# Performance work log

Measured on AMD Instinct MI355X. Metric: run time of the kernel, lower is better.

## Reference

```python
import jax, jax.numpy as jnp
import numpy as np

N = 100000  # nodes
E = 1600000  # directed edges

_DIMS = [("eg1", 3, 160), ("eg2", 160, 80), ("eg3", 80, 40), ("eg4", 40, 20),
         ("el1", 20, 10), ("el2", 10, 3), ("dl1", 3, 10), ("dl2", 10, 20),
         ("dg1", 20, 40), ("dg2", 40, 80), ("dg3", 80, 160), ("dg4", 160, 3)]


def _lin_init(key, ci, co):
    s = 1.0 / np.sqrt(ci)
    kw, kb = jax.random.split(key)
    w = jax.random.uniform(kw, (ci, co), jnp.float32, -s, s)
    b = jax.random.uniform(kb, (co,), jnp.float32, -s, s)
    return w, b


def setup_inputs():
    key = jax.random.key(0)
    k0, k1, k2 = jax.random.split(key, 3)
    x = jax.random.normal(k0, (N, 3), jnp.float32)
    src = jax.random.randint(k1, (E,), 0, N)
    dst = jax.random.randint(k2, (E,), 0, N)
    edge_index = jnp.stack([src, dst])  # [2, E] int32 indices
    out = {"x": x, "edge_index": edge_index}
    for i, (name, ci, co) in enumerate(_DIMS):
        w, b = _lin_init(jax.random.fold_in(key, i + 10), ci, co)
        out[name + "_w"] = w
        out[name + "_b"] = b
    return out


def _gcn(x, w, b, src, dst, norm):
    # PyG GCNConv: linear transform, then symmetric-normalized scatter-add.
    h = x @ w
    agg = jax.ops.segment_sum(h[src] * norm[:, None], dst, num_segments=N)
    return agg + b


def reference(x, edge_index, eg1_w, eg1_b, eg2_w, eg2_b, eg3_w, eg3_b, eg4_w, eg4_b,
              el1_w, el1_b, el2_w, el2_b, dl1_w, dl1_b, dl2_w, dl2_b,
              dg1_w, dg1_b, dg2_w, dg2_b, dg3_w, dg3_b, dg4_w, dg4_b):
    loops = jnp.arange(N)
    src = jnp.concatenate([edge_index[0], loops])  # add self-loops (PyG default)
    dst = jnp.concatenate([edge_index[1], loops])
    deg = jax.ops.segment_sum(jnp.ones(src.shape[0], x.dtype), dst, num_segments=N)
    dis = jnp.where(deg > 0, jax.lax.rsqrt(deg), 0.0)
    norm = dis[src] * dis[dst]  # D^-1/2 A D^-1/2 edge weights
    relu = jax.nn.relu
    h = relu(_gcn(x, eg1_w, eg1_b, src, dst, norm))
    h = relu(_gcn(h, eg2_w, eg2_b, src, dst, norm))
    h = relu(_gcn(h, eg3_w, eg3_b, src, dst, norm))
    h = relu(_gcn(h, eg4_w, eg4_b, src, dst, norm))
    h = relu(h @ el1_w + el1_b)
    h = h @ el2_w + el2_b  # latent [N, 3]
    h = relu(h @ dl1_w + dl1_b)
    h = relu(h @ dl2_w + dl2_b)
    h = relu(_gcn(h, dg1_w, dg1_b, src, dst, norm))
    h = relu(_gcn(h, dg2_w, dg2_b, src, dst, norm))
    h = relu(_gcn(h, dg3_w, dg3_b, src, dst, norm))
    h = jnp.tanh(_gcn(h, dg4_w, dg4_b, src, dst, norm))
    return h
```

## Files before the change

### kernel.cpp

```cpp
#include <hip/hip_runtime.h>
#include <hip/hip_fp16.h>
#include <math.h>

#define BS 256
static constexpr int NN = 100000;
static constexpr int EE = 1600000;
static constexpr int BUCKET_SH = 7;
static constexpr int NBUCKET = (NN + 127) >> BUCKET_SH;
static constexpr int NB_PART = 256;
static constexpr int CHUNK = EE / NB_PART;
static constexpr int NP_ = NBUCKET * NB_PART;
static constexpr int SCAN_ELEMS = 1024;
static constexpr int NPB = (NP_ + SCAN_ELEMS - 1) / SCAN_ELEMS;

static inline int cdiv(long long a, int b) { return (int)((a + b - 1) / b); }

typedef _Float16 half8 __attribute__((ext_vector_type(8)));
typedef float f32x4 __attribute__((ext_vector_type(4)));

template <int ACT>
__device__ __forceinline__ float act_f(float v) {
    if (ACT == 1) return fmaxf(v, 0.0f);
    if (ACT == 2) return tanhf(v);
    return v;
}

__device__ __forceinline__ unsigned short h16(float v) {
    return __half_as_ushort(__float2half(v));
}
__device__ __forceinline__ unsigned pack2h(float a, float b) {
    return (unsigned)h16(a) | ((unsigned)h16(b) << 16);
}
__device__ __forceinline__ float4 cvt4h(uint2 r) {
    float2 fa = __half22float2(*(const __half2*)&r.x);
    float2 fb = __half22float2(*(const __half2*)&r.y);
    return make_float4(fa.x, fa.y, fb.x, fb.y);
}
__device__ __forceinline__ void acc8h(uint4 r, float4& a, float4& b) {
    float2 f0 = __half22float2(*(const __half2*)&r.x);
    float2 f1 = __half22float2(*(const __half2*)&r.y);
    float2 f2 = __half22float2(*(const __half2*)&r.z);
    float2 f3 = __half22float2(*(const __half2*)&r.w);
    a.x += f0.x; a.y += f0.y; a.z += f1.x; a.w += f1.y;
    b.x += f2.x; b.y += f2.y; b.z += f3.x; b.w += f3.y;
}

template <int OUTM>
__device__ __forceinline__ void store1(float* out, size_t idx, float v, float dn) {
    if (OUTM == 0) out[idx] = v;
    else if (OUTM == 1) out[idx] = v * dn;
    else if (OUTM == 2) ((unsigned short*)out)[idx] = h16(v * dn);
    else ((unsigned short*)out)[idx] = h16(v);
}

__global__ __launch_bounds__(256) void k_hist(const int* __restrict__ dst,
                                              int* __restrict__ part_cnt) {
    __shared__ int h[NBUCKET];
    int b = blockIdx.x;
    for (int j = threadIdx.x; j < NBUCKET; j += 256) h[j] = 0;
    __syncthreads();
    int e0 = b * CHUNK;
    for (int k = threadIdx.x; k < CHUNK; k += 256)
        atomicAdd(&h[dst[e0 + k] >> BUCKET_SH], 1);
    __syncthreads();
    for (int j = threadIdx.x; j < NBUCKET; j += 256)
        part_cnt[j * NB_PART + b] = h[j];
}

__global__ void k_scanA(const int* __restrict__ in, int* __restrict__ outp,
                        int* __restrict__ bsums) {
    __shared__ int lds[BS];
    int base = blockIdx.x * SCAN_ELEMS;
    int t = threadIdx.x;
    int v[4];
    int s = 0;
#pragma unroll
    for (int j = 0; j < 4; ++j) {
        int idx = base + t * 4 + j;
        v[j] = (idx < NP_) ? in[idx] : 0;
        s += v[j];
    }
    lds[t] = s;
    __syncthreads();
    for (int off = 1; off < BS; off <<= 1) {
        int add = (t >= off) ? lds[t - off] : 0;
        __syncthreads();
        lds[t] += add;
        __syncthreads();
    }
    int run = lds[t] - s;
    if (t == BS - 1) bsums[blockIdx.x] = lds[BS - 1];
#pragma unroll
    for (int j = 0; j < 4; ++j) {
        int idx = base + t * 4 + j;
        if (idx < NP_) outp[idx] = run;
        run += v[j];
    }
}

__global__ void k_scanB(int* __restrict__ bsums) {
    if (threadIdx.x == 0 && blockIdx.x == 0) {
        int acc = 0;
        for (int i = 0; i < NPB; ++i) {
            int t = bsums[i];
            bsums[i] = acc;
            acc += t;
        }
    }
}

__global__ void k_scanC(int* __restrict__ outp, const int* __restrict__ bsums,
                        int* __restrict__ bbase) {
    int i = blockIdx.x * BS + threadIdx.x;
    if (i < NP_) {
        int v = outp[i] + bsums[i / SCAN_ELEMS];
        outp[i] = v;
        if ((i & (NB_PART - 1)) == 0) bbase[i / NB_PART] = v;
    }
    if (i == 0) bbase[NBUCKET] = EE;
}

__global__ __launch_bounds__(256) void k_part(const int* __restrict__ src,
                                              const int* __restrict__ dst,
                                              const int* __restrict__ scan_out,
                                              unsigned* __restrict__ epb) {
    __shared__ int cur[NBUCKET];
    int b = blockIdx.x;
    for (int j = threadIdx.x; j < NBUCKET; j += 256) cur[j] = scan_out[j * NB_PART + b];
    __syncthreads();
    int e0 = b * CHUNK;
    for (int k = threadIdx.x; k < CHUNK; k += 256) {
        int e = e0 + k;
        int d = dst[e];
        int s = src[e];
        int pos = atomicAdd(&cur[d >> BUCKET_SH], 1);
        epb[pos] = ((unsigned)(d & ((1 << BUCKET_SH) - 1)) << 17) | (unsigned)s;
    }
}

__global__ __launch_bounds__(256) void k_fine2(const int* __restrict__ bbase,
                                               const unsigned* __restrict__ epb,
                                               int* __restrict__ eidx,
                                               int* __restrict__ rowptr,
                                               float* __restrict__ dis) {
    __shared__ int hcnt[1 << BUCKET_SH];
    __shared__ int hoff[1 << BUCKET_SH];
    int b = blockIdx.x;
    int n0 = b << BUCKET_SH;
    int nloc = min(1 << BUCKET_SH, NN - n0);
    int t = threadIdx.x;
    if (t < (1 << BUCKET_SH)) hcnt[t] = 0;
    __syncthreads();
    int es = bbase[b], ee = bbase[b + 1];
    for (int k = es + t; k < ee; k += 256) atomicAdd(&hcnt[epb[k] >> 17], 1);
    __syncthreads();
    if (t < (1 << BUCKET_SH)) hoff[t] = hcnt[t];
    __syncthreads();
    for (int off = 1; off < (1 << BUCKET_SH); off <<= 1) {
        int add = (t >= off && t < (1 << BUCKET_SH)) ? hoff[t - off] : 0;
        __syncthreads();
        if (t < (1 << BUCKET_SH)) hoff[t] += add;
        __syncthreads();
    }
    if (t < nloc) {
        int excl = hoff[t] - hcnt[t];
        rowptr[n0 + t] = es + excl;
        dis[n0 + t] = rsqrtf((float)(hcnt[t] + 1));
    }
    __syncthreads();
    if (t < (1 << BUCKET_SH)) hoff[t] = es + hoff[t] - hcnt[t];
    __syncthreads();
    for (int k = es + t; k < ee; k += 256) {
        unsigned p = epb[k];
        int pos = atomicAdd(&hoff[p >> 17], 1);
        eidx[pos] = (int)(p & 0x1FFFFu);
    }
    if (b == NBUCKET - 1 && t == 0) rowptr[NN] = EE;
}

template <int C, int ACT, bool HASB, bool OUTH>
__global__ void k_gatherw(const unsigned short* __restrict__ g, const int* __restrict__ rowptr,
                          const int* __restrict__ eidx, const float* __restrict__ dis,
                          const float* __restrict__ b, float* __restrict__ out) {
    static_assert(C % 8 == 0, "C%8");
    constexpr int V = C / 8;
    int t = blockIdx.x * BS + threadIdx.x;
    if (t >= NN * V) return;
    int n = t / V, v = t % V;
    const uint4* g4 = (const uint4*)g;
    float4 accA = make_float4(0.f, 0.f, 0.f, 0.f);
    float4 accB = make_float4(0.f, 0.f, 0.f, 0.f);
    acc8h(g4[(size_t)n * V + v], accA, accB);
    int rs = rowptr[n], re = rowptr[n + 1];
    int k = rs;
    for (; k + 4 <= re; k += 4) {
        int s0 = eidx[k + 0], s1 = eidx[k + 1], s2 = eidx[k + 2], s3 = eidx[k + 3];
        uint4 r0 = g4[(size_t)s0 * V + v];
        uint4 r1 = g4[(size_t)s1 * V + v];
        uint4 r2 = g4[(size_t)s2 * V + v];
        uint4 r3 = g4[(size_t)s3 * V + v];
        acc8h(r0, accA, accB);
        acc8h(r1, accA, accB);
        acc8h(r2, accA, accB);
        acc8h(r3, accA, accB);
    }
    for (; k < re; ++k) {
        acc8h(g4[(size_t)eidx[k] * V + v], accA, accB);
    }
    float dn = dis[n];
    accA.x *= dn; accA.y *= dn; accA.z *= dn; accA.w *= dn;
    accB.x *= dn; accB.y *= dn; accB.z *= dn; accB.w *= dn;
    if (HASB) {
        float4 b0 = ((const float4*)b)[v * 2 + 0];
        float4 b1 = ((const float4*)b)[v * 2 + 1];
        accA.x += b0.x; accA.y += b0.y; accA.z += b0.z; accA.w += b0.w;
        accB.x += b1.x; accB.y += b1.y; accB.z += b1.z; accB.w += b1.w;
    }
    accA.x = act_f<ACT>(accA.x); accA.y = act_f<ACT>(accA.y);
    accA.z = act_f<ACT>(accA.z); accA.w = act_f<ACT>(accA.w);
    accB.x = act_f<ACT>(accB.x); accB.y = act_f<ACT>(accB.y);
    accB.z = act_f<ACT>(accB.z); accB.w = act_f<ACT>(accB.w);
    if (OUTH) {
        uint4 u;
        u.x = pack2h(accA.x, accA.y);
        u.y = pack2h(accA.z, accA.w);
        u.z = pack2h(accB.x, accB.y);
        u.w = pack2h(accB.z, accB.w);
        ((uint4*)out)[(size_t)n * V + v] = u;
    } else {
        float4* op = (float4*)out + (size_t)n * (C / 4) + v * 2;
        op[0] = accA;
        op[1] = accB;
    }
}

template <int C, int ACT, bool HASB, bool OUTH>
__global__ void k_gatherh(const unsigned short* __restrict__ g, const int* __restrict__ rowptr,
                          const int* __restrict__ eidx, const float* __restrict__ dis,
                          const float* __restrict__ b, float* __restrict__ out) {
    static_assert(C % 4 == 0, "C%4");
    constexpr int V = C / 4;
    int t = blockIdx.x * BS + threadIdx.x;
    if (t >= NN * V) return;
    int n = t / V, v = t % V;
    const uint2* g2 = (const uint2*)g;
    float4 acc = cvt4h(g2[(size_t)n * V + v]);
    int rs = rowptr[n], re = rowptr[n + 1];
    int k = rs;
    for (; k + 4 <= re; k += 4) {
        int s0 = eidx[k + 0], s1 = eidx[k + 1], s2 = eidx[k + 2], s3 = eidx[k + 3];
        uint2 r0 = g2[(size_t)s0 * V + v];
        uint2 r1 = g2[(size_t)s1 * V + v];
        uint2 r2 = g2[(size_t)s2 * V + v];
        uint2 r3 = g2[(size_t)s3 * V + v];
        float4 h0 = cvt4h(r0), h1 = cvt4h(r1), h2 = cvt4h(r2), h3 = cvt4h(r3);
        acc.x += (h0.x + h1.x) + (h2.x + h3.x);
        acc.y += (h0.y + h1.y) + (h2.y + h3.y);
        acc.z += (h0.z + h1.z) + (h2.z + h3.z);
        acc.w += (h0.w + h1.w) + (h2.w + h3.w);
    }
    for (; k < re; ++k) {
        float4 hv = cvt4h(g2[(size_t)eidx[k] * V + v]);
        acc.x += hv.x; acc.y += hv.y; acc.z += hv.z; acc.w += hv.w;
    }
    float dn = dis[n];
    acc.x *= dn; acc.y *= dn; acc.z *= dn; acc.w *= dn;
    if (HASB) {
        float4 bb = ((const float4*)b)[v];
        acc.x += bb.x; acc.y += bb.y; acc.z += bb.z; acc.w += bb.w;
    }
    acc.x = act_f<ACT>(acc.x);
    acc.y = act_f<ACT>(acc.y);
    acc.z = act_f<ACT>(acc.z);
    acc.w = act_f<ACT>(acc.w);
    if (OUTH) {
        uint2 u;
        u.x = pack2h(acc.x, acc.y);
        u.y = pack2h(acc.z, acc.w);
        ((uint2*)out)[(size_t)n * V + v] = u;
    } else {
        ((float4*)out)[(size_t)n * V + v] = acc;
    }
}

template <int ACT, bool HASB>
__global__ void k_gather3d(const float* __restrict__ g, const int* __restrict__ rowptr,
                           const int* __restrict__ eidx, const float* __restrict__ dis,
                           const float* __restrict__ b, float* __restrict__ out) {
    int n = blockIdx.x * BS + threadIdx.x;
    if (n >= NN) return;
    const float* gp = g + (size_t)n * 3;
    float a0 = gp[0], a1 = gp[1], a2 = gp[2];
    int rs = rowptr[n], re = rowptr[n + 1];
    int k = rs;
    for (; k + 4 <= re; k += 4) {
        const float* q0 = g + (size_t)eidx[k + 0] * 3;
        const float* q1 = g + (size_t)eidx[k + 1] * 3;
        const float* q2 = g + (size_t)eidx[k + 2] * 3;
        const float* q3 = g + (size_t)eidx[k + 3] * 3;
        float b00 = q0[0], b01 = q0[1], b02 = q0[2];
        float b10 = q1[0], b11 = q1[1], b12 = q1[2];
        float b20 = q2[0], b21 = q2[1], b22 = q2[2];
        float b30 = q3[0], b31 = q3[1], b32 = q3[2];
        a0 += (b00 + b10) + (b20 + b30);
        a1 += (b01 + b11) + (b21 + b31);
        a2 += (b02 + b12) + (b22 + b32);
    }
    for (; k < re; ++k) {
        const float* gq = g + (size_t)eidx[k] * 3;
        a0 += gq[0]; a1 += gq[1]; a2 += gq[2];
    }
    float dn = dis[n];
    a0 *= dn; a1 *= dn; a2 *= dn;
    if (HASB) { a0 += b[0]; a1 += b[1]; a2 += b[2]; }
    float* op = out + (size_t)n * 3;
    op[0] = act_f<ACT>(a0);
    op[1] = act_f<ACT>(a1);
    op[2] = act_f<ACT>(a2);
}

__global__ void k_scale3(const float* __restrict__ x, const float* __restrict__ dis,
                         float* __restrict__ g) {
    int i = blockIdx.x * BS + threadIdx.x;
    if (i < NN * 3) g[i] = x[i] * dis[i / 3];
}

__global__ __launch_bounds__(256) void k_latent(const unsigned short* __restrict__ in20,
                                                const float* __restrict__ el1_w, const float* __restrict__ el1_b,
                                                const float* __restrict__ el2_w, const float* __restrict__ el2_b,
                                                const float* __restrict__ dl1_w, const float* __restrict__ dl1_b,
                                                const float* __restrict__ dl2_w, const float* __restrict__ dl2_b,
                                                const float* __restrict__ dis,
                                                unsigned short* __restrict__ G) {
    __shared__ float w1[200], b1[10], w2[30], b2[3], w3[30], b3[10], w4[200], b4[20];
    int t = threadIdx.x;
    if (t < 200) w1[t] = el1_w[t];
    if (t < 10) b1[t] = el1_b[t];
    if (t < 30) w2[t] = el2_w[t];
    if (t < 3) b2[t] = el2_b[t];
    if (t < 30) w3[t] = dl1_w[t];
    if (t < 10) b3[t] = dl1_b[t];
    if (t < 200) w4[t] = dl2_w[t];
    if (t < 20) b4[t] = dl2_b[t];
    __syncthreads();
    int n = blockIdx.x * 256 + t;
    if (n >= NN) return;
    float h0[20];
    const uint2* ip = (const uint2*)in20 + (size_t)n * 5;
#pragma unroll
    for (int v = 0; v < 5; ++v) {
        float4 f = cvt4h(ip[v]);
        h0[v * 4 + 0] = f.x; h0[v * 4 + 1] = f.y;
        h0[v * 4 + 2] = f.z; h0[v * 4 + 3] = f.w;
    }
    float a1[10];
#pragma unroll
    for (int j = 0; j < 10; ++j) {
        float s = b1[j];
#pragma unroll
        for (int i = 0; i < 20; ++i) s = fmaf(h0[i], w1[i * 10 + j], s);
        a1[j] = fmaxf(s, 0.0f);
    }
    float a2[3];
#pragma unroll
    for (int j = 0; j < 3; ++j) {
        float s = b2[j];
#pragma unroll
        for (int i = 0; i < 10; ++i) s = fmaf(a1[i], w2[i * 3 + j], s);
        a2[j] = s;
    }
    float a3[10];
#pragma unroll
    for (int j = 0; j < 10; ++j) {
        float s = b3[j];
#pragma unroll
        for (int i = 0; i < 3; ++i) s = fmaf(a2[i], w3[i * 10 + j], s);
        a3[j] = fmaxf(s, 0.0f);
    }
    float dn = dis[n];
    uint2* gp = (uint2*)G + (size_t)n * 5;
#pragma unroll
    for (int v = 0; v < 5; ++v) {
        float o[4];
#pragma unroll
        for (int q = 0; q < 4; ++q) {
            int j = v * 4 + q;
            float s = b4[j];
#pragma unroll
            for (int i = 0; i < 10; ++i) s = fmaf(a3[i], w4[i * 20 + j], s);
            o[q] = fmaxf(s, 0.0f) * dn;
        }
        uint2 u;
        u.x = pack2h(o[0], o[1]);
        u.y = pack2h(o[2], o[3]);
        gp[v] = u;
    }
}

template <int K, int N>
__global__ void k_wprep(const float* __restrict__ w, _Float16* __restrict__ wh) {
    constexpr int KP = (K + 31) & ~31;
    constexpr int NT = (N + 15) / 16;
    constexpr int NPAD = NT * 16;
    int i = blockIdx.x * 256 + threadIdx.x;
    if (i >= KP * NPAD) return;
    int k = i / NPAD, n = i % NPAD;
    float v = (k < K && n < N) ? w[k * N + n] : 0.0f;
    wh[((size_t)(k >> 3) * NPAD + n) * 8 + (k & 7)] = (_Float16)v;
}

template <int K, int N, int ACT, bool HASB, int OUTM>
__global__ __launch_bounds__(256) void k_mfma(const unsigned short* __restrict__ x,
                                              const _Float16* __restrict__ wh,
                                              const float* __restrict__ bias,
                                              unsigned short* __restrict__ out,
                                              const float* __restrict__ dis) {
    static_assert(K % 8 == 0, "K%8");
    constexpr int KP = (K + 31) & ~31;
    constexpr int KC = KP / 32;
    constexpr int NT = (N + 15) / 16;
    constexpr int NPAD = NT * 16;
    const int wid = blockIdx.x * 4 + (threadIdx.x >> 6);
    const int lane = threadIdx.x & 63;
    const int lm = lane & 15;
    const int quad = lane >> 4;
    const int arow = wid * 16 + lm;

    f32x4 acc[NT];
#pragma unroll
    for (int t = 0; t < NT; ++t) acc[t] = (f32x4){0.f, 0.f, 0.f, 0.f};

    const _Float16* xr = (const _Float16*)x + (size_t)arow * K;
#pragma unroll
    for (int kc = 0; kc < KC; ++kc) {
        int k0 = kc * 32 + quad * 8;
        half8 a = (half8)(_Float16)0;
        if (arow < NN && k0 < K) a = *(const half8*)(xr + k0);
#pragma unroll
        for (int t = 0; t < NT; ++t) {
            half8 bf = *(const half8*)&wh[((size_t)(kc * 4 + quad) * NPAD + t * 16 + lm) * 8];
            acc[t] = __builtin_amdgcn_mfma_f32_16x16x32_f16(a, bf, acc[t], 0, 0, 0);
        }
    }

    float bb[NT];
#pragma unroll
    for (int t = 0; t < NT; ++t) {
        int col = t * 16 + lm;
        bb[t] = (HASB && col < N) ? bias[col] : 0.0f;
    }
#pragma unroll
    for (int r = 0; r < 4; ++r) {
        int orow = wid * 16 + quad * 4 + r;
        if (orow < NN) {
            float dn = (OUTM == 2) ? dis[orow] : 1.0f;
#pragma unroll
            for (int t = 0; t < NT; ++t) {
                int col = t * 16 + lm;
                if (col < N) {
                    float v = act_f<ACT>(acc[t][r] + bb[t]);
                    if (OUTM == 2) v *= dn;
                    out[(size_t)orow * N + col] = h16(v);
                }
            }
        }
    }
}

template <int CIN, int COUT, int ACT, int OUTM>
__global__ void k_mm_rowbcast(const float* __restrict__ x, const float* __restrict__ w,
                              const float* __restrict__ b, float* __restrict__ out) {
    static_assert(COUT % 4 == 0, "c4");
    constexpr int COUT4 = COUT / 4;
    int i = blockIdx.x * BS + threadIdx.x;
    if (i >= NN * COUT4) return;
    int n = i / COUT4, c4 = i % COUT4;
    const float4* w4 = (const float4*)w;
    float4 acc = ((const float4*)b)[c4];
    const float* xr = x + (size_t)n * CIN;
#pragma unroll
    for (int ci = 0; ci < CIN; ++ci) {
        float xv = xr[ci];
        float4 wv = w4[ci * COUT4 + c4];
        acc.x = fmaf(xv, wv.x, acc.x);
        acc.y = fmaf(xv, wv.y, acc.y);
        acc.z = fmaf(xv, wv.z, acc.z);
        acc.w = fmaf(xv, wv.w, acc.w);
    }
    acc.x = act_f<ACT>(acc.x); acc.y = act_f<ACT>(acc.y);
    acc.z = act_f<ACT>(acc.z); acc.w = act_f<ACT>(acc.w);
    if (OUTM == 3) {
        uint2 u;
        u.x = pack2h(acc.x, acc.y);
        u.y = pack2h(acc.z, acc.w);
        ((uint2*)out)[(size_t)n * COUT4 + c4] = u;
    } else {
        ((float4*)out)[(size_t)n * COUT4 + c4] = acc;
    }
}

template <int CIN, int COUT, int ACT, bool HASB, int OUTM, bool INH>
__global__ void k_mm_vec4(const float* __restrict__ x, const float* __restrict__ w,
                          const float* __restrict__ b, float* __restrict__ out,
                          const float* __restrict__ dis) {
    static_assert(CIN % 4 == 0 && COUT % 4 == 0, "align");
    constexpr int TM = 8;
    constexpr int CIN4 = CIN / 4;
    constexpr int COUT4 = COUT / 4;
    constexpr int RG = NN / TM;
    int i = blockIdx.x * BS + threadIdx.x;
    if (i >= RG * COUT4) return;
    int c4 = i % COUT4;
    int n0 = (i / COUT4) * TM;
    const float4* x4 = (const float4*)x;
    const uint2* xh = (const uint2*)x;
    const float4* w4 = (const float4*)w;
    float4 acc[TM];
    float4 bb = HASB ? ((const float4*)b)[c4] : make_float4(0.f, 0.f, 0.f, 0.f);
#pragma unroll
    for (int r = 0; r < TM; ++r) acc[r] = bb;
    for (int k4 = 0; k4 < CIN4; ++k4) {
        float4 wv[4];
#pragma unroll
        for (int j = 0; j < 4; ++j) wv[j] = w4[(size_t)(4 * k4 + j) * COUT4 + c4];
#pragma unroll
        for (int r = 0; r < TM; ++r) {
            float4 xv;
            if (INH) xv = cvt4h(xh[(size_t)(n0 + r) * CIN4 + k4]);
            else xv = x4[(size_t)(n0 + r) * CIN4 + k4];
            acc[r].x = fmaf(xv.x, wv[0].x, fmaf(xv.y, wv[1].x, fmaf(xv.z, wv[2].x, fmaf(xv.w, wv[3].x, acc[r].x))));
            acc[r].y = fmaf(xv.x, wv[0].y, fmaf(xv.y, wv[1].y, fmaf(xv.z, wv[2].y, fmaf(xv.w, wv[3].y, acc[r].y))));
            acc[r].z = fmaf(xv.x, wv[0].z, fmaf(xv.y, wv[1].z, fmaf(xv.z, wv[2].z, fmaf(xv.w, wv[3].z, acc[r].z))));
            acc[r].w = fmaf(xv.x, wv[0].w, fmaf(xv.y, wv[1].w, fmaf(xv.z, wv[2].w, fmaf(xv.w, wv[3].w, acc[r].w))));
        }
    }
#pragma unroll
    for (int r = 0; r < TM; ++r) {
        float vx = act_f<ACT>(acc[r].x), vy = act_f<ACT>(acc[r].y);
        float vz = act_f<ACT>(acc[r].z), vw = act_f<ACT>(acc[r].w);
        size_t gi = (size_t)(n0 + r) * COUT4 + c4;
        if (OUTM == 2) {
            float dn = dis[n0 + r];
            uint2 u;
            u.x = pack2h(vx * dn, vy * dn);
            u.y = pack2h(vz * dn, vw * dn);
            ((uint2*)out)[gi] = u;
        } else if (OUTM == 1) {
            float dn = dis[n0 + r];
            ((float4*)out)[gi] = make_float4(vx * dn, vy * dn, vz * dn, vw * dn);
        } else {
            ((float4*)out)[gi] = make_float4(vx, vy, vz, vw);
        }
    }
}

template <int CIN, int COUT, int ACT, bool HASB, int OUTM, bool INH>
__global__ void k_mm_vec(const float* __restrict__ x, const float* __restrict__ w,
                         const float* __restrict__ b, float* __restrict__ out,
                         const float* __restrict__ dis) {
    static_assert(CIN % 4 == 0, "CIN%4");
    constexpr int TM = 8;
    constexpr int CIN4 = CIN / 4;
    constexpr int RG = NN / TM;
    int i = blockIdx.x * BS + threadIdx.x;
    if (i >= RG * COUT) return;
    int c = i % COUT;
    int n0 = (i / COUT) * TM;
    float acc[TM];
    float bb = HASB ? b[c] : 0.0f;
#pragma unroll
    for (int r = 0; r < TM; ++r) acc[r] = bb;
    const float4* x4 = (const float4*)x;
    const uint2* xh = (const uint2*)x;
    for (int k = 0; k < CIN4; ++k) {
        float w0 = w[(4 * k + 0) * COUT + c];
        float w1 = w[(4 * k + 1) * COUT + c];
        float w2 = w[(4 * k + 2) * COUT + c];
        float w3 = w[(4 * k + 3) * COUT + c];
#pragma unroll
        for (int r = 0; r < TM; ++r) {
            float4 xv;
            if (INH) xv = cvt4h(xh[(size_t)(n0 + r) * CIN4 + k]);
            else xv = x4[(size_t)(n0 + r) * CIN4 + k];
            acc[r] = fmaf(xv.x, w0, fmaf(xv.y, w1, fmaf(xv.z, w2, fmaf(xv.w, w3, acc[r]))));
        }
    }
#pragma unroll
    for (int r = 0; r < TM; ++r) {
        int row = n0 + r;
        float dn = (OUTM == 1 || OUTM == 2) ? dis[row] : 0.0f;
        store1<OUTM>(out, (size_t)row * COUT + c, act_f<ACT>(acc[r]), dn);
    }
}

extern "C" void kernel_launch(void* const* d_in, const int* in_sizes, int n_in,
                              void* d_out, int out_size, void* d_ws, size_t ws_size,
                              hipStream_t stream) {
    const float* x = (const float*)d_in[0];
    const int* ei = (const int*)d_in[1];
    const int* src = ei;
    const int* dst = ei + EE;
    const float* eg1_w = (const float*)d_in[2];  const float* eg1_b = (const float*)d_in[3];
    const float* eg2_w = (const float*)d_in[4];  const float* eg2_b = (const float*)d_in[5];
    const float* eg3_w = (const float*)d_in[6];  const float* eg3_b = (const float*)d_in[7];
    const float* eg4_w = (const float*)d_in[8];  const float* eg4_b = (const float*)d_in[9];
    const float* el1_w = (const float*)d_in[10]; const float* el1_b = (const float*)d_in[11];
    const float* el2_w = (const float*)d_in[12]; const float* el2_b = (const float*)d_in[13];
    const float* dl1_w = (const float*)d_in[14]; const float* dl1_b = (const float*)d_in[15];
    const float* dl2_w = (const float*)d_in[16]; const float* dl2_b = (const float*)d_in[17];
    const float* dg1_w = (const float*)d_in[18]; const float* dg1_b = (const float*)d_in[19];
    const float* dg2_w = (const float*)d_in[20]; const float* dg2_b = (const float*)d_in[21];
    const float* dg3_w = (const float*)d_in[22]; const float* dg3_b = (const float*)d_in[23];
    const float* dg4_w = (const float*)d_in[24]; const float* dg4_b = (const float*)d_in[25];
    float* out = (float*)d_out;

    char* ws = (char*)d_ws;
    size_t off = 0;
    auto alloc = [&](size_t bytes) {
        void* p = ws + off;
        off += (bytes + 15) & ~(size_t)15;
        return p;
    };
    int* part_cnt = (int*)alloc(sizeof(int) * NP_);
    int* scan_out = (int*)alloc(sizeof(int) * NP_);
    int* bsums    = (int*)alloc(sizeof(int) * NPB);
    int* bbase    = (int*)alloc(sizeof(int) * (NBUCKET + 1));
    int* rowptr   = (int*)alloc(sizeof(int) * (NN + 1));
    float* dis    = (float*)alloc(sizeof(float) * NN);
    int* eidx     = (int*)alloc(sizeof(int) * EE);
    unsigned* epb = (unsigned*)alloc(sizeof(unsigned) * EE);
    unsigned short* G = (unsigned short*)alloc(sizeof(unsigned short) * 80 * (size_t)NN);
    float* bufA = (float*)alloc(sizeof(float) * 160 * (size_t)NN);
    float* bufB = (float*)alloc(sizeof(float) * 160 * (size_t)NN);
    _Float16* whEg2 = (_Float16*)alloc(sizeof(_Float16) * (160 / 8) * 80 * 8);
    _Float16* whEg3 = (_Float16*)alloc(sizeof(_Float16) * (96 / 8) * 48 * 8);
    _Float16* whDg2 = (_Float16*)alloc(sizeof(_Float16) * (64 / 8) * 80 * 8);
    _Float16* whDg3 = (_Float16*)alloc(sizeof(_Float16) * (96 / 8) * 160 * 8);

    k_hist<<<NB_PART, 256, 0, stream>>>(dst, part_cnt);
    k_scanA<<<NPB, BS, 0, stream>>>(part_cnt, scan_out, bsums);
    k_scanB<<<1, 64, 0, stream>>>(bsums);
    k_scanC<<<cdiv(NP_, BS), BS, 0, stream>>>(scan_out, bsums, bbase);
    k_part<<<NB_PART, 256, 0, stream>>>(src, dst, scan_out, epb);
    k_fine2<<<NBUCKET, 256, 0, stream>>>(bbase, epb, eidx, rowptr, dis);

    k_wprep<160, 80><<<cdiv(160 * 80, 256), 256, 0, stream>>>(eg2_w, whEg2);
    k_wprep<80, 40><<<cdiv(96 * 48, 256), 256, 0, stream>>>(eg3_w, whEg3);
    k_wprep<40, 80><<<cdiv(64 * 80, 256), 256, 0, stream>>>(dg2_w, whDg2);
    k_wprep<80, 160><<<cdiv(96 * 160, 256), 256, 0, stream>>>(dg3_w, whDg3);

    k_scale3<<<cdiv(3LL * NN, BS), BS, 0, stream>>>(x, dis, bufB);
    k_gather3d<0, false><<<cdiv(NN, BS), BS, 0, stream>>>(bufB, rowptr, eidx, dis, nullptr, bufA);
    k_mm_rowbcast<3, 160, 1, 3><<<cdiv(NN * 40LL, BS), BS, 0, stream>>>(bufA, eg1_w, eg1_b, bufB);

    k_mfma<160, 80, 0, false, 2><<<cdiv(NN, 64), 256, 0, stream>>>(
        (const unsigned short*)bufB, whEg2, nullptr, G, dis);
    k_gatherw<80, 1, true, true><<<cdiv(NN * 10LL, BS), BS, 0, stream>>>(G, rowptr, eidx, dis, eg2_b, bufA);

    k_mfma<80, 40, 0, false, 2><<<cdiv(NN, 64), 256, 0, stream>>>(
        (const unsigned short*)bufA, whEg3, nullptr, G, dis);
    k_gatherw<40, 1, true, true><<<cdiv(NN * 5LL, BS), BS, 0, stream>>>(G, rowptr, eidx, dis, eg3_b, bufB);

    k_mm_vec4<40, 20, 0, false, 2, true><<<cdiv((NN / 8) * 5LL, BS), BS, 0, stream>>>(
        bufB, eg4_w, nullptr, (float*)G, dis);
    k_gatherh<20, 1, true, true><<<cdiv(NN * 5LL, BS), BS, 0, stream>>>(G, rowptr, eidx, dis, eg4_b, bufA);

    k_latent<<<cdiv(NN, 256), 256, 0, stream>>>((const unsigned short*)bufA,
        el1_w, el1_b, el2_w, el2_b, dl1_w, dl1_b, dl2_w, dl2_b, dis, G);

    k_gatherh<20, 0, false, true><<<cdiv(NN * 5LL, BS), BS, 0, stream>>>(G, rowptr, eidx, dis, nullptr, bufA);
    k_mm_vec4<20, 40, 1, true, 2, true><<<cdiv((NN / 8) * 10LL, BS), BS, 0, stream>>>(
        bufA, dg1_w, dg1_b, (float*)G, dis);

    k_gatherw<40, 0, false, true><<<cdiv(NN * 5LL, BS), BS, 0, stream>>>(G, rowptr, eidx, dis, nullptr, bufB);
    k_mfma<40, 80, 1, true, 2><<<cdiv(NN, 64), 256, 0, stream>>>(
        (const unsigned short*)bufB, whDg2, dg2_b, G, dis);

    k_gatherw<80, 0, false, true><<<cdiv(NN * 10LL, BS), BS, 0, stream>>>(G, rowptr, eidx, dis, nullptr, bufA);
    k_mfma<80, 160, 1, true, 3><<<cdiv(NN, 64), 256, 0, stream>>>(
        (const unsigned short*)bufA, whDg3, dg3_b, (unsigned short*)bufB, nullptr);

    k_mm_vec<160, 3, 0, false, 1, true><<<cdiv((NN / 8) * 3LL, BS), BS, 0, stream>>>(bufB, dg4_w, nullptr, bufA, dis);
    k_gather3d<2, true><<<cdiv(NN, BS), BS, 0, stream>>>(bufA, rowptr, eidx, dis, dg4_b, out);
}
```

Measured before the change: 527.4 us.

## Fuse neighbor gathers with following matmuls into combined per-layer kernels

```diff
diff --git a/kernel.cpp b/kernel.cpp
--- a/kernel.cpp
+++ b/kernel.cpp
@@ -43,6 +43,19 @@
     float2 f3 = __half22float2(*(const __half2*)&r.w);
     a.x += f0.x; a.y += f0.y; a.z += f1.x; a.w += f1.y;
     b.x += f2.x; b.y += f2.y; b.z += f3.x; b.w += f3.y;
+}
+__device__ __forceinline__ void addrow8(uint4 r, float* h) {
+    float2 f0 = __half22float2(*(const __half2*)&r.x);
+    float2 f1 = __half22float2(*(const __half2*)&r.y);
+    float2 f2 = __half22float2(*(const __half2*)&r.z);
+    float2 f3 = __half22float2(*(const __half2*)&r.w);
+    h[0] += f0.x; h[1] += f0.y; h[2] += f1.x; h[3] += f1.y;
+    h[4] += f2.x; h[5] += f2.y; h[6] += f3.x; h[7] += f3.y;
+}
+__device__ __forceinline__ void addrow4(uint2 r, float* h) {
+    float2 f0 = __half22float2(*(const __half2*)&r.x);
+    float2 f1 = __half22float2(*(const __half2*)&r.y);
+    h[0] += f0.x; h[1] += f0.y; h[2] += f1.x; h[3] += f1.y;
 }
 
 template <int OUTM>
@@ -178,109 +191,54 @@
     if (b == NBUCKET - 1 && t == 0) rowptr[NN] = EE;
 }
 
-template <int C, int ACT, bool HASB, bool OUTH>
-__global__ void k_gatherw(const unsigned short* __restrict__ g, const int* __restrict__ rowptr,
-                          const int* __restrict__ eidx, const float* __restrict__ dis,
-                          const float* __restrict__ b, float* __restrict__ out) {
-    static_assert(C % 8 == 0, "C%8");
-    constexpr int V = C / 8;
-    int t = blockIdx.x * BS + threadIdx.x;
-    if (t >= NN * V) return;
-    int n = t / V, v = t % V;
-    const uint4* g4 = (const uint4*)g;
-    float4 accA = make_float4(0.f, 0.f, 0.f, 0.f);
-    float4 accB = make_float4(0.f, 0.f, 0.f, 0.f);
-    acc8h(g4[(size_t)n * V + v], accA, accB);
+template <int K, int N>
+__device__ __forceinline__ void wconv(const float* __restrict__ w, _Float16* __restrict__ wh, int i) {
+    constexpr int NT = (N + 15) / 16;
+    constexpr int NPAD = NT * 16;
+    int k = i / NPAD, n = i % NPAD;
+    float v = (k < K && n < N) ? w[k * N + n] : 0.0f;
+    wh[((size_t)(k >> 3) * NPAD + n) * 8 + (k & 7)] = (_Float16)v;
+}
+
+__global__ void k_wprep_all(const float* __restrict__ w1, const float* __restrict__ w2,
+                            const float* __restrict__ w3, const float* __restrict__ w4,
+                            _Float16* __restrict__ o1, _Float16* __restrict__ o2,
+                            _Float16* __restrict__ o3, _Float16* __restrict__ o4) {
+    int i = blockIdx.x * 256 + threadIdx.x;
+    if (i < 12800) wconv<160, 80>(w1, o1, i);
+    else if (i < 17408) wconv<80, 40>(w2, o2, i - 12800);
+    else if (i < 22528) wconv<40, 80>(w3, o3, i - 17408);
+    else if (i < 37888) wconv<80, 160>(w4, o4, i - 22528);
+}
+
+__global__ void k_gather3x(const float* __restrict__ x, const int* __restrict__ rowptr,
+                           const int* __restrict__ eidx, const float* __restrict__ dis,
+                           float* __restrict__ out) {
+    int n = blockIdx.x * BS + threadIdx.x;
+    if (n >= NN) return;
+    float dn = dis[n];
+    float a0 = x[(size_t)n * 3 + 0] * dn;
+    float a1 = x[(size_t)n * 3 + 1] * dn;
+    float a2 = x[(size_t)n * 3 + 2] * dn;
     int rs = rowptr[n], re = rowptr[n + 1];
     int k = rs;
-    for (; k + 4 <= re; k += 4) {
-        int s0 = eidx[k + 0], s1 = eidx[k + 1], s2 = eidx[k + 2], s3 = eidx[k + 3];
-        uint4 r0 = g4[(size_t)s0 * V + v];
-        uint4 r1 = g4[(size_t)s1 * V + v];
-        uint4 r2 = g4[(size_t)s2 * V + v];
-        uint4 r3 = g4[(size_t)s3 * V + v];
-        acc8h(r0, accA, accB);
-        acc8h(r1, accA, accB);
-        acc8h(r2, accA, accB);
-        acc8h(r3, accA, accB);
+    for (; k + 2 <= re; k += 2) {
+        int s0 = eidx[k], s1 = eidx[k + 1];
+        float d0 = dis[s0], d1 = dis[s1];
+        const float* q0 = x + (size_t)s0 * 3;
+        const float* q1 = x + (size_t)s1 * 3;
+        a0 += q0[0] * d0 + q1[0] * d1;
+        a1 += q0[1] * d0 + q1[1] * d1;
+        a2 += q0[2] * d0 + q1[2] * d1;
     }
     for (; k < re; ++k) {
-        acc8h(g4[(size_t)eidx[k] * V + v], accA, accB);
-    }
-    float dn = dis[n];
-    accA.x *= dn; accA.y *= dn; accA.z *= dn; accA.w *= dn;
-    accB.x *= dn; accB.y *= dn; accB.z *= dn; accB.w *= dn;
-    if (HASB) {
-        float4 b0 = ((const float4*)b)[v * 2 + 0];
-        float4 b1 = ((const float4*)b)[v * 2 + 1];
-        accA.x += b0.x; accA.y += b0.y; accA.z += b0.z; accA.w += b0.w;
-        accB.x += b1.x; accB.y += b1.y; accB.z += b1.z; accB.w += b1.w;
-    }
-    accA.x = act_f<ACT>(accA.x); accA.y = act_f<ACT>(accA.y);
-    accA.z = act_f<ACT>(accA.z); accA.w = act_f<ACT>(accA.w);
-    accB.x = act_f<ACT>(accB.x); accB.y = act_f<ACT>(accB.y);
-    accB.z = act_f<ACT>(accB.z); accB.w = act_f<ACT>(accB.w);
-    if (OUTH) {
-        uint4 u;
-        u.x = pack2h(accA.x, accA.y);
-        u.y = pack2h(accA.z, accA.w);
-        u.z = pack2h(accB.x, accB.y);
-        u.w = pack2h(accB.z, accB.w);
-        ((uint4*)out)[(size_t)n * V + v] = u;
-    } else {
-        float4* op = (float4*)out + (size_t)n * (C / 4) + v * 2;
-        op[0] = accA;
-        op[1] = accB;
-    }
-}
-
-template <int C, int ACT, bool HASB, bool OUTH>
-__global__ void k_gatherh(const unsigned short* __restrict__ g, const int* __restrict__ rowptr,
-                          const int* __restrict__ eidx, const float* __restrict__ dis,
-                          const float* __restrict__ b, float* __restrict__ out) {
-    static_assert(C % 4 == 0, "C%4");
-    constexpr int V = C / 4;
-    int t = blockIdx.x * BS + threadIdx.x;
-    if (t >= NN * V) return;
-    int n = t / V, v = t % V;
-    const uint2* g2 = (const uint2*)g;
-    float4 acc = cvt4h(g2[(size_t)n * V + v]);
-    int rs = rowptr[n], re = rowptr[n + 1];
-    int k = rs;
-    for (; k + 4 <= re; k += 4) {
-        int s0 = eidx[k + 0], s1 = eidx[k + 1], s2 = eidx[k + 2], s3 = eidx[k + 3];
-        uint2 r0 = g2[(size_t)s0 * V + v];
-        uint2 r1 = g2[(size_t)s1 * V + v];
-        uint2 r2 = g2[(size_t)s2 * V + v];
-        uint2 r3 = g2[(size_t)s3 * V + v];
-        float4 h0 = cvt4h(r0), h1 = cvt4h(r1), h2 = cvt4h(r2), h3 = cvt4h(r3);
-        acc.x += (h0.x + h1.x) + (h2.x + h3.x);
-        acc.y += (h0.y + h1.y) + (h2.y + h3.y);
-        acc.z += (h0.z + h1.z) + (h2.z + h3.z);
-        acc.w += (h0.w + h1.w) + (h2.w + h3.w);
-    }
-    for (; k < re; ++k) {
-        float4 hv = cvt4h(g2[(size_t)eidx[k] * V + v]);
-        acc.x += hv.x; acc.y += hv.y; acc.z += hv.z; acc.w += hv.w;
-    }
-    float dn = dis[n];
-    acc.x *= dn; acc.y *= dn; acc.z *= dn; acc.w *= dn;
-    if (HASB) {
-        float4 bb = ((const float4*)b)[v];
-        acc.x += bb.x; acc.y += bb.y; acc.z += bb.z; acc.w += bb.w;
-    }
-    acc.x = act_f<ACT>(acc.x);
-    acc.y = act_f<ACT>(acc.y);
-    acc.z = act_f<ACT>(acc.z);
-    acc.w = act_f<ACT>(acc.w);
-    if (OUTH) {
-        uint2 u;
-        u.x = pack2h(acc.x, acc.y);
-        u.y = pack2h(acc.z, acc.w);
-        ((uint2*)out)[(size_t)n * V + v] = u;
-    } else {
-        ((float4*)out)[(size_t)n * V + v] = acc;
-    }
+        int s = eidx[k];
+        float ds = dis[s];
+        const float* q = x + (size_t)s * 3;
+        a0 += q[0] * ds; a1 += q[1] * ds; a2 += q[2] * ds;
+    }
+    float* op = out + (size_t)n * 3;
+    op[0] = a0 * dn; op[1] = a1 * dn; op[2] = a2 * dn;
 }
 
 template <int ACT, bool HASB>
@@ -298,13 +256,9 @@
         const float* q1 = g + (size_t)eidx[k + 1] * 3;
         const float* q2 = g + (size_t)eidx[k + 2] * 3;
         const float* q3 = g + (size_t)eidx[k + 3] * 3;
-        float b00 = q0[0], b01 = q0[1], b02 = q0[2];
-        float b10 = q1[0], b11 = q1[1], b12 = q1[2];
-        float b20 = q2[0], b21 = q2[1], b22 = q2[2];
-        float b30 = q3[0], b31 = q3[1], b32 = q3[2];
-        a0 += (b00 + b10) + (b20 + b30);
-        a1 += (b01 + b11) + (b21 + b31);
-        a2 += (b02 + b12) + (b22 + b32);
+        a0 += (q0[0] + q1[0]) + (q2[0] + q3[0]);
+        a1 += (q0[1] + q1[1]) + (q2[1] + q3[1]);
+        a2 += (q0[2] + q1[2]) + (q2[2] + q3[2]);
     }
     for (; k < re; ++k) {
         const float* gq = g + (size_t)eidx[k] * 3;
@@ -319,20 +273,241 @@
     op[2] = act_f<ACT>(a2);
 }
 
-__global__ void k_scale3(const float* __restrict__ x, const float* __restrict__ dis,
-                         float* __restrict__ g) {
-    int i = blockIdx.x * BS + threadIdx.x;
-    if (i < NN * 3) g[i] = x[i] * dis[i / 3];
-}
-
-__global__ __launch_bounds__(256) void k_latent(const unsigned short* __restrict__ in20,
-                                                const float* __restrict__ el1_w, const float* __restrict__ el1_b,
-                                                const float* __restrict__ el2_w, const float* __restrict__ el2_b,
-                                                const float* __restrict__ dl1_w, const float* __restrict__ dl1_b,
-                                                const float* __restrict__ dl2_w, const float* __restrict__ dl2_b,
-                                                const float* __restrict__ dis,
-                                                unsigned short* __restrict__ G) {
-    __shared__ float w1[200], b1[10], w2[30], b2[3], w3[30], b3[10], w4[200], b4[20];
+__global__ __launch_bounds__(256) void k_eg12(const float* __restrict__ a3,
+                                              const float* __restrict__ w1,
+                                              const float* __restrict__ b1,
+                                              const _Float16* __restrict__ wh2,
+                                              unsigned short* __restrict__ out,
+                                              const float* __restrict__ dis) {
+    constexpr int SP = 168;
+    __shared__ _Float16 Al[64 * SP];
+    __shared__ float xs[192];
+    __shared__ float w1s[480];
+    __shared__ float b1s[160];
+    const int tid = threadIdx.x;
+    const int n0 = blockIdx.x * 64;
+    for (int i = tid; i < 192; i += 256) {
+        int n = n0 + i / 3;
+        xs[i] = (n < NN) ? a3[(size_t)n0 * 3 + i] : 0.0f;
+    }
+    for (int i = tid; i < 480; i += 256) w1s[i] = w1[i];
+    if (tid < 160) b1s[tid] = b1[tid];
+    __syncthreads();
+    for (int i = tid; i < 64 * 160; i += 256) {
+        int r = i / 160, c = i % 160;
+        float v = b1s[c] + xs[r * 3 + 0] * w1s[c] + xs[r * 3 + 1] * w1s[160 + c] +
+                  xs[r * 3 + 2] * w1s[320 + c];
+        Al[r * SP + c] = (_Float16)fmaxf(v, 0.0f);
+    }
+    __syncthreads();
+    const int wave = tid >> 6, lane = tid & 63;
+    const int lm = lane & 15, quad = lane >> 4;
+    f32x4 acc[5];
+#pragma unroll
+    for (int t = 0; t < 5; ++t) acc[t] = (f32x4){0.f, 0.f, 0.f, 0.f};
+    const int arow = wave * 16 + lm;
+#pragma unroll
+    for (int kc = 0; kc < 5; ++kc) {
+        half8 a = *(const half8*)&Al[arow * SP + kc * 32 + quad * 8];
+#pragma unroll
+        for (int t = 0; t < 5; ++t) {
+            half8 bf = *(const half8*)&wh2[((size_t)(kc * 4 + quad) * 80 + t * 16 + lm) * 8];
+            acc[t] = __builtin_amdgcn_mfma_f32_16x16x32_f16(a, bf, acc[t], 0, 0, 0);
+        }
+    }
+#pragma unroll
+    for (int r = 0; r < 4; ++r) {
+        int orow = n0 + wave * 16 + quad * 4 + r;
+        if (orow < NN) {
+            float dn = dis[orow];
+#pragma unroll
+            for (int t = 0; t < 5; ++t) {
+                int col = t * 16 + lm;
+                out[(size_t)orow * 80 + col] = h16(acc[t][r] * dn);
+            }
+        }
+    }
+}
+
+template <int CIN, int COUT, bool GHASB, int GACT, bool MHASB, int MACT, int OUTM>
+__global__ __launch_bounds__(256) void k_gmfma(const unsigned short* __restrict__ gin,
+                                               const int* __restrict__ rowptr,
+                                               const int* __restrict__ eidx,
+                                               const float* __restrict__ dis,
+                                               const float* __restrict__ gbias,
+                                               const _Float16* __restrict__ wh,
+                                               const float* __restrict__ mbias,
+                                               unsigned short* __restrict__ out) {
+    static_assert(CIN % 8 == 0, "CIN%8");
+    constexpr int V = CIN / 8;
+    constexpr int SP = CIN + 8;
+    constexpr int KP = (CIN + 31) & ~31;
+    constexpr int KC = KP / 32;
+    constexpr int NT = (COUT + 15) / 16;
+    constexpr int NPAD = NT * 16;
+    __shared__ _Float16 Al[64 * SP];
+    const int tid = threadIdx.x;
+    const int n0 = blockIdx.x * 64;
+    const uint4* g4 = (const uint4*)gin;
+
+    for (int i = tid; i < 64 * V; i += 256) {
+        int r = i / V, c8 = i % V;
+        int n = n0 + r;
+        half8 hv = (half8)(_Float16)0;
+        if (n < NN) {
+            float4 aA = make_float4(0.f, 0.f, 0.f, 0.f);
+            float4 aB = make_float4(0.f, 0.f, 0.f, 0.f);
+            acc8h(g4[(size_t)n * V + c8], aA, aB);
+            int rs = rowptr[n], re = rowptr[n + 1];
+            int k = rs;
+            for (; k + 4 <= re; k += 4) {
+                int s0 = eidx[k + 0], s1 = eidx[k + 1], s2 = eidx[k + 2], s3 = eidx[k + 3];
+                uint4 r0 = g4[(size_t)s0 * V + c8];
+                uint4 r1 = g4[(size_t)s1 * V + c8];
+                uint4 r2 = g4[(size_t)s2 * V + c8];
+                uint4 r3 = g4[(size_t)s3 * V + c8];
+                acc8h(r0, aA, aB);
+                acc8h(r1, aA, aB);
+                acc8h(r2, aA, aB);
+                acc8h(r3, aA, aB);
+            }
+            for (; k < re; ++k) acc8h(g4[(size_t)eidx[k] * V + c8], aA, aB);
+            float dn = dis[n];
+            aA.x *= dn; aA.y *= dn; aA.z *= dn; aA.w *= dn;
+            aB.x *= dn; aB.y *= dn; aB.z *= dn; aB.w *= dn;
+            if (GHASB) {
+                float4 b0 = ((const float4*)gbias)[c8 * 2 + 0];
+                float4 b1 = ((const float4*)gbias)[c8 * 2 + 1];
+                aA.x += b0.x; aA.y += b0.y; aA.z += b0.z; aA.w += b0.w;
+                aB.x += b1.x; aB.y += b1.y; aB.z += b1.z; aB.w += b1.w;
+            }
+            if (GACT == 1) {
+                aA.x = fmaxf(aA.x, 0.f); aA.y = fmaxf(aA.y, 0.f);
+                aA.z = fmaxf(aA.z, 0.f); aA.w = fmaxf(aA.w, 0.f);
+                aB.x = fmaxf(aB.x, 0.f); aB.y = fmaxf(aB.y, 0.f);
+                aB.z = fmaxf(aB.z, 0.f); aB.w = fmaxf(aB.w, 0.f);
+            }
+            hv[0] = (_Float16)aA.x; hv[1] = (_Float16)aA.y;
+            hv[2] = (_Float16)aA.z; hv[3] = (_Float16)aA.w;
+            hv[4] = (_Float16)aB.x; hv[5] = (_Float16)aB.y;
+            hv[6] = (_Float16)aB.z; hv[7] = (_Float16)aB.w;
+        }
+        *(half8*)&Al[r * SP + c8 * 8] = hv;
+    }
+    __syncthreads();
+
+    const int wave = tid >> 6, lane = tid & 63;
+    const int lm = lane & 15, quad = lane >> 4;
+    f32x4 acc[NT];
+#pragma unroll
+    for (int t = 0; t < NT; ++t) acc[t] = (f32x4){0.f, 0.f, 0.f, 0.f};
+    const int arow = wave * 16 + lm;
+#pragma unroll
+    for (int kc = 0; kc < KC; ++kc) {
+        int k0 = kc * 32 + quad * 8;
+        half8 a = (half8)(_Float16)0;
+        if (k0 < CIN) a = *(const half8*)&Al[arow * SP + k0];
+#pragma unroll
+        for (int t = 0; t < NT; ++t) {
+            half8 bf = *(const half8*)&wh[((size_t)(kc * 4 + quad) * NPAD + t * 16 + lm) * 8];
+            acc[t] = __builtin_amdgcn_mfma_f32_16x16x32_f16(a, bf, acc[t], 0, 0, 0);
+        }
+    }
+    float bb[NT];
+#pragma unroll
+    for (int t = 0; t < NT; ++t) {
+        int col = t * 16 + lm;
+        bb[t] = (MHASB && col < COUT) ? mbias[col] : 0.0f;
+    }
+#pragma unroll
+    for (int r = 0; r < 4; ++r) {
+        int orow = n0 + wave * 16 + quad * 4 + r;
+        if (orow < NN) {
+            float dn = (OUTM == 2) ? dis[orow] : 1.0f;
+#pragma unroll
+            for (int t = 0; t < NT; ++t) {
+                int col = t * 16 + lm;
+                if (col < COUT) {
+                    float v = act_f<MACT>(acc[t][r] + bb[t]);
+                    if (OUTM == 2) v *= dn;
+                    out[(size_t)orow * COUT + col] = h16(v);
+                }
+            }
+        }
+    }
+}
+
+__global__ __launch_bounds__(256) void k_g40mm(const unsigned short* __restrict__ gin,
+                                               const int* __restrict__ rowptr,
+                                               const int* __restrict__ eidx,
+                                               const float* __restrict__ dis,
+                                               const float* __restrict__ gb,
+                                               const float* __restrict__ w,
+                                               unsigned short* __restrict__ out) {
+    __shared__ float wS[800];
+    __shared__ float bS[40];
+    int tid = threadIdx.x;
+    for (int i = tid; i < 800; i += 256) wS[i] = w[i];
+    if (tid < 40) bS[tid] = gb[tid];
+    __syncthreads();
+    int n = blockIdx.x * 256 + tid;
+    if (n >= NN) return;
+    const uint4* g4 = (const uint4*)gin;
+    float h[40];
+#pragma unroll
+    for (int i = 0; i < 40; ++i) h[i] = 0.0f;
+#pragma unroll
+    for (int c8 = 0; c8 < 5; ++c8) addrow8(g4[(size_t)n * 5 + c8], &h[c8 * 8]);
+    int rs = rowptr[n], re = rowptr[n + 1];
+    int k = rs;
+    for (; k + 2 <= re; k += 2) {
+        int s0 = eidx[k], s1 = eidx[k + 1];
+#pragma unroll
+        for (int c8 = 0; c8 < 5; ++c8) {
+            uint4 r0 = g4[(size_t)s0 * 5 + c8];
+            uint4 r1 = g4[(size_t)s1 * 5 + c8];
+            addrow8(r0, &h[c8 * 8]);
+            addrow8(r1, &h[c8 * 8]);
+        }
+    }
+    for (; k < re; ++k) {
+        int s = eidx[k];
+#pragma unroll
+        for (int c8 = 0; c8 < 5; ++c8) addrow8(g4[(size_t)s * 5 + c8], &h[c8 * 8]);
+    }
+    float dn = dis[n];
+#pragma unroll
+    for (int i = 0; i < 40; ++i) h[i] = fmaxf(h[i] * dn + bS[i], 0.0f);
+    float z[20];
+#pragma unroll
+    for (int j = 0; j < 20; ++j) z[j] = 0.0f;
+#pragma unroll
+    for (int i = 0; i < 40; ++i) {
+        float hv = h[i];
+#pragma unroll
+        for (int j = 0; j < 20; ++j) z[j] = fmaf(hv, wS[i * 20 + j], z[j]);
+    }
+    uint2* gp = (uint2*)out + (size_t)n * 5;
+#pragma unroll
+    for (int q = 0; q < 5; ++q) {
+        uint2 u;
+        u.x = pack2h(z[q * 4 + 0] * dn, z[q * 4 + 1] * dn);
+        u.y = pack2h(z[q * 4 + 2] * dn, z[q * 4 + 3] * dn);
+        gp[q] = u;
+    }
+}
+
+__global__ __launch_bounds__(256) void k_g20_latent(const unsigned short* __restrict__ gin,
+                                                    const int* __restrict__ rowptr,
+                                                    const int* __restrict__ eidx,
+                                                    const float* __restrict__ dis,
+                                                    const float* __restrict__ gb,
+                                                    const float* __restrict__ el1_w, const float* __restrict__ el1_b,
+                                                    const float* __restrict__ el2_w, const float* __restrict__ el2_b,
+                                                    const float* __restrict__ dl1_w, const float* __restrict__ dl1_b,
+                                                    const float* __restrict__ dl2_w, const float* __restrict__ dl2_b,
+                                                    unsigned short* __restrict__ out) {
+    __shared__ float w1[200], b1[10], w2[30], b2[3], w3[30], b3[10], w4[200], b4[20], bg[20];
     int t = threadIdx.x;
     if (t < 200) w1[t] = el1_w[t];
     if (t < 10) b1[t] = el1_b[t];
@@ -342,17 +517,40 @@
     if (t < 10) b3[t] = dl1_b[t];
     if (t < 200) w4[t] = dl2_w[t];
     if (t < 20) b4[t] = dl2_b[t];
+    if (t >= 220 && t < 240) bg[t - 220] = gb[t - 220];
     __syncthreads();
     int n = blockIdx.x * 256 + t;
     if (n >= NN) return;
+    const uint2* g2 = (const uint2*)gin;
     float h0[20];
-    const uint2* ip = (const uint2*)in20 + (size_t)n * 5;
-#pragma unroll
-    for (int v = 0; v < 5; ++v) {
-        float4 f = cvt4h(ip[v]);
-        h0[v * 4 + 0] = f.x; h0[v * 4 + 1] = f.y;
-        h0[v * 4 + 2] = f.z; h0[v * 4 + 3] = f.w;
-    }
+#pragma unroll
+    for (int i = 0; i < 20; ++i) h0[i] = 0.0f;
+#pragma unroll
+    for (int c4 = 0; c4 < 5; ++c4) addrow4(g2[(size_t)n * 5 + c4], &h0[c4 * 4]);
+    int rs = rowptr[n], re = rowptr[n + 1];
+    int k = rs;
+    for (; k + 4 <= re; k += 4) {
+        int s0 = eidx[k], s1 = eidx[k + 1], s2 = eidx[k + 2], s3 = eidx[k + 3];
+#pragma unroll
+        for (int c4 = 0; c4 < 5; ++c4) {
+            uint2 r0 = g2[(size_t)s0 * 5 + c4];
+            uint2 r1 = g2[(size_t)s1 * 5 + c4];
+            uint2 r2 = g2[(size_t)s2 * 5 + c4];
+            uint2 r3 = g2[(size_t)s3 * 5 + c4];
+            addrow4(r0, &h0[c4 * 4]);
+            addrow4(r1, &h0[c4 * 4]);
+            addrow4(r2, &h0[c4 * 4]);
+            addrow4(r3, &h0[c4 * 4]);
+        }
+    }
+    for (; k < re; ++k) {
+        int s = eidx[k];
+#pragma unroll
+        for (int c4 = 0; c4 < 5; ++c4) addrow4(g2[(size_t)s * 5 + c4], &h0[c4 * 4]);
+    }
+    float dn = dis[n];
+#pragma unroll
+    for (int i = 0; i < 20; ++i) h0[i] = fmaxf(h0[i] * dn + bg[i], 0.0f);
     float a1[10];
 #pragma unroll
     for (int j = 0; j < 10; ++j) {
@@ -377,8 +575,7 @@
         for (int i = 0; i < 3; ++i) s = fmaf(a2[i], w3[i * 10 + j], s);
         a3[j] = fmaxf(s, 0.0f);
     }
-    float dn = dis[n];
-    uint2* gp = (uint2*)G + (size_t)n * 5;
+    uint2* gp = (uint2*)out + (size_t)n * 5;
 #pragma unroll
     for (int v = 0; v < 5; ++v) {
         float o[4];
@@ -397,160 +594,71 @@
     }
 }
 
-template <int K, int N>
-__global__ void k_wprep(const float* __restrict__ w, _Float16* __restrict__ wh) {
-    constexpr int KP = (K + 31) & ~31;
-    constexpr int NT = (N + 15) / 16;
-    constexpr int NPAD = NT * 16;
-    int i = blockIdx.x * 256 + threadIdx.x;
-    if (i >= KP * NPAD) return;
-    int k = i / NPAD, n = i % NPAD;
-    float v = (k < K && n < N) ? w[k * N + n] : 0.0f;
-    wh[((size_t)(k >> 3) * NPAD + n) * 8 + (k & 7)] = (_Float16)v;
-}
-
-template <int K, int N, int ACT, bool HASB, int OUTM>
-__global__ __launch_bounds__(256) void k_mfma(const unsigned short* __restrict__ x,
-                                              const _Float16* __restrict__ wh,
-                                              const float* __restrict__ bias,
-                                              unsigned short* __restrict__ out,
-                                              const float* __restrict__ dis) {
-    static_assert(K % 8 == 0, "K%8");
-    constexpr int KP = (K + 31) & ~31;
-    constexpr int KC = KP / 32;
-    constexpr int NT = (N + 15) / 16;
-    constexpr int NPAD = NT * 16;
-    const int wid = blockIdx.x * 4 + (threadIdx.x >> 6);
-    const int lane = threadIdx.x & 63;
-    const int lm = lane & 15;
-    const int quad = lane >> 4;
-    const int arow = wid * 16 + lm;
-
-    f32x4 acc[NT];
-#pragma unroll
-    for (int t = 0; t < NT; ++t) acc[t] = (f32x4){0.f, 0.f, 0.f, 0.f};
-
-    const _Float16* xr = (const _Float16*)x + (size_t)arow * K;
-#pragma unroll
-    for (int kc = 0; kc < KC; ++kc) {
-        int k0 = kc * 32 + quad * 8;
-        half8 a = (half8)(_Float16)0;
-        if (arow < NN && k0 < K) a = *(const half8*)(xr + k0);
-#pragma unroll
-        for (int t = 0; t < NT; ++t) {
-            half8 bf = *(const half8*)&wh[((size_t)(kc * 4 + quad) * NPAD + t * 16 + lm) * 8];
-            acc[t] = __builtin_amdgcn_mfma_f32_16x16x32_f16(a, bf, acc[t], 0, 0, 0);
-        }
-    }
-
-    float bb[NT];
-#pragma unroll
-    for (int t = 0; t < NT; ++t) {
-        int col = t * 16 + lm;
-        bb[t] = (HASB && col < N) ? bias[col] : 0.0f;
-    }
-#pragma unroll
-    for (int r = 0; r < 4; ++r) {
-        int orow = wid * 16 + quad * 4 + r;
-        if (orow < NN) {
-            float dn = (OUTM == 2) ? dis[orow] : 1.0f;
-#pragma unroll
-            for (int t = 0; t < NT; ++t) {
-                int col = t * 16 + lm;
-                if (col < N) {
-                    float v = act_f<ACT>(acc[t][r] + bb[t]);
-                    if (OUTM == 2) v *= dn;
-                    out[(size_t)orow * N + col] = h16(v);
-                }
-            }
-        }
-    }
-}
-
-template <int CIN, int COUT, int ACT, int OUTM>
-__global__ void k_mm_rowbcast(const float* __restrict__ x, const float* __restrict__ w,
-                              const float* __restrict__ b, float* __restrict__ out) {
-    static_assert(COUT % 4 == 0, "c4");
-    constexpr int COUT4 = COUT / 4;
-    int i = blockIdx.x * BS + threadIdx.x;
-    if (i >= NN * COUT4) return;
-    int n = i / COUT4, c4 = i % COUT4;
-    const float4* w4 = (const float4*)w;
-    float4 acc = ((const float4*)b)[c4];
-    const float* xr = x + (size_t)n * CIN;
-#pragma unroll
-    for (int ci = 0; ci < CIN; ++ci) {
-        float xv = xr[ci];
-        float4 wv = w4[ci * COUT4 + c4];
-        acc.x = fmaf(xv, wv.x, acc.x);
-        acc.y = fmaf(xv, wv.y, acc.y);
-        acc.z = fmaf(xv, wv.z, acc.z);
-        acc.w = fmaf(xv, wv.w, acc.w);
-    }
-    acc.x = act_f<ACT>(acc.x); acc.y = act_f<ACT>(acc.y);
-    acc.z = act_f<ACT>(acc.z); acc.w = act_f<ACT>(acc.w);
-    if (OUTM == 3) {
+__global__ __launch_bounds__(256) void k_g20_mm(const unsigned short* __restrict__ gin,
+                                                const int* __restrict__ rowptr,
+                                                const int* __restrict__ eidx,
+                                                const float* __restrict__ dis,
+                                                const float* __restrict__ w,
+                                                const float* __restrict__ b,
+                                                unsigned short* __restrict__ out) {
+    __shared__ float wS[800];
+    __shared__ float bS[40];
+    int tid = threadIdx.x;
+    for (int i = tid; i < 800; i += 256) wS[i] = w[i];
+    if (tid < 40) bS[tid] = b[tid];
+    __syncthreads();
+    int n = blockIdx.x * 256 + tid;
+    if (n >= NN) return;
+    const uint2* g2 = (const uint2*)gin;
+    float h[20];
+#pragma unroll
+    for (int i = 0; i < 20; ++i) h[i] = 0.0f;
+#pragma unroll
+    for (int c4 = 0; c4 < 5; ++c4) addrow4(g2[(size_t)n * 5 + c4], &h[c4 * 4]);
+    int rs = rowptr[n], re = rowptr[n + 1];
+    int k = rs;
+    for (; k + 4 <= re; k += 4) {
+        int s0 = eidx[k], s1 = eidx[k + 1], s2 = eidx[k + 2], s3 = eidx[k + 3];
+#pragma unroll
+        for (int c4 = 0; c4 < 5; ++c4) {
+            uint2 r0 = g2[(size_t)s0 * 5 + c4];
+            uint2 r1 = g2[(size_t)s1 * 5 + c4];
+            uint2 r2 = g2[(size_t)s2 * 5 + c4];
+            uint2 r3 = g2[(size_t)s3 * 5 + c4];
+            addrow4(r0, &h[c4 * 4]);
+            addrow4(r1, &h[c4 * 4]);
+            addrow4(r2, &h[c4 * 4]);
+            addrow4(r3, &h[c4 * 4]);
+        }
+    }
+    for (; k < re; ++k) {
+        int s = eidx[k];
+#pragma unroll
+        for (int c4 = 0; c4 < 5; ++c4) addrow4(g2[(size_t)s * 5 + c4], &h[c4 * 4]);
+    }
+    float dn = dis[n];
+#pragma unroll
+    for (int i = 0; i < 20; ++i) h[i] *= dn;
+    float z[40];
+#pragma unroll
+    for (int j = 0; j < 40; ++j) z[j] = bS[j];
+#pragma unroll
+    for (int i = 0; i < 20; ++i) {
+        float hv = h[i];
+#pragma unroll
+        for (int j = 0; j < 40; ++j) z[j] = fmaf(hv, wS[i * 40 + j], z[j]);
+    }
+    uint2* gp = (uint2*)out + (size_t)n * 10;
+#pragma unroll
+    for (int q = 0; q < 10; ++q) {
+        float z0 = fmaxf(z[q * 4 + 0], 0.f) * dn;
+        float z1 = fmaxf(z[q * 4 + 1], 0.f) * dn;
+        float z2 = fmaxf(z[q * 4 + 2], 0.f) * dn;
+        float z3 = fmaxf(z[q * 4 + 3], 0.f) * dn;
         uint2 u;
-        u.x = pack2h(acc.x, acc.y);
-        u.y = pack2h(acc.z, acc.w);
-        ((uint2*)out)[(size_t)n * COUT4 + c4] = u;
-    } else {
-        ((float4*)out)[(size_t)n * COUT4 + c4] = acc;
-    }
-}
-
-template <int CIN, int COUT, int ACT, bool HASB, int OUTM, bool INH>
-__global__ void k_mm_vec4(const float* __restrict__ x, const float* __restrict__ w,
-                          const float* __restrict__ b, float* __restrict__ out,
-                          const float* __restrict__ dis) {
-    static_assert(CIN % 4 == 0 && COUT % 4 == 0, "align");
-    constexpr int TM = 8;
-    constexpr int CIN4 = CIN / 4;
-    constexpr int COUT4 = COUT / 4;
-    constexpr int RG = NN / TM;
-    int i = blockIdx.x * BS + threadIdx.x;
-    if (i >= RG * COUT4) return;
-    int c4 = i % COUT4;
-    int n0 = (i / COUT4) * TM;
-    const float4* x4 = (const float4*)x;
-    const uint2* xh = (const uint2*)x;
-    const float4* w4 = (const float4*)w;
-    float4 acc[TM];
-    float4 bb = HASB ? ((const float4*)b)[c4] : make_float4(0.f, 0.f, 0.f, 0.f);
-#pragma unroll
-    for (int r = 0; r < TM; ++r) acc[r] = bb;
-    for (int k4 = 0; k4 < CIN4; ++k4) {
-        float4 wv[4];
-#pragma unroll
-        for (int j = 0; j < 4; ++j) wv[j] = w4[(size_t)(4 * k4 + j) * COUT4 + c4];
-#pragma unroll
-        for (int r = 0; r < TM; ++r) {
-            float4 xv;
-            if (INH) xv = cvt4h(xh[(size_t)(n0 + r) * CIN4 + k4]);
-            else xv = x4[(size_t)(n0 + r) * CIN4 + k4];
-            acc[r].x = fmaf(xv.x, wv[0].x, fmaf(xv.y, wv[1].x, fmaf(xv.z, wv[2].x, fmaf(xv.w, wv[3].x, acc[r].x))));
-            acc[r].y = fmaf(xv.x, wv[0].y, fmaf(xv.y, wv[1].y, fmaf(xv.z, wv[2].y, fmaf(xv.w, wv[3].y, acc[r].y))));
-            acc[r].z = fmaf(xv.x, wv[0].z, fmaf(xv.y, wv[1].z, fmaf(xv.z, wv[2].z, fmaf(xv.w, wv[3].z, acc[r].z))));
-            acc[r].w = fmaf(xv.x, wv[0].w, fmaf(xv.y, wv[1].w, fmaf(xv.z, wv[2].w, fmaf(xv.w, wv[3].w, acc[r].w))));
-        }
-    }
-#pragma unroll
-    for (int r = 0; r < TM; ++r) {
-        float vx = act_f<ACT>(acc[r].x), vy = act_f<ACT>(acc[r].y);
-        float vz = act_f<ACT>(acc[r].z), vw = act_f<ACT>(acc[r].w);
-        size_t gi = (size_t)(n0 + r) * COUT4 + c4;
-        if (OUTM == 2) {
-            float dn = dis[n0 + r];
-            uint2 u;
-            u.x = pack2h(vx * dn, vy * dn);
-            u.y = pack2h(vz * dn, vw * dn);
-            ((uint2*)out)[gi] = u;
-        } else if (OUTM == 1) {
-            float dn = dis[n0 + r];
-            ((float4*)out)[gi] = make_float4(vx * dn, vy * dn, vz * dn, vw * dn);
-        } else {
-            ((float4*)out)[gi] = make_float4(vx, vy, vz, vw);
-        }
+        u.x = pack2h(z0, z1);
+        u.y = pack2h(z2, z3);
+        gp[q] = u;
     }
 }
 
@@ -629,13 +737,14 @@
     float* dis    = (float*)alloc(sizeof(float) * NN);
     int* eidx     = (int*)alloc(sizeof(int) * EE);
     unsigned* epb = (unsigned*)alloc(sizeof(unsigned) * EE);
-    unsigned short* G = (unsigned short*)alloc(sizeof(unsigned short) * 80 * (size_t)NN);
-    float* bufA = (float*)alloc(sizeof(float) * 160 * (size_t)NN);
-    float* bufB = (float*)alloc(sizeof(float) * 160 * (size_t)NN);
-    _Float16* whEg2 = (_Float16*)alloc(sizeof(_Float16) * (160 / 8) * 80 * 8);
-    _Float16* whEg3 = (_Float16*)alloc(sizeof(_Float16) * (96 / 8) * 48 * 8);
-    _Float16* whDg2 = (_Float16*)alloc(sizeof(_Float16) * (64 / 8) * 80 * 8);
-    _Float16* whDg3 = (_Float16*)alloc(sizeof(_Float16) * (96 / 8) * 160 * 8);
+    float* A3     = (float*)alloc(sizeof(float) * 3 * (size_t)NN);
+    unsigned short* GA = (unsigned short*)alloc(sizeof(unsigned short) * 80 * (size_t)NN);
+    unsigned short* GB = (unsigned short*)alloc(sizeof(unsigned short) * 80 * (size_t)NN);
+    unsigned short* B160 = (unsigned short*)alloc(sizeof(unsigned short) * 160 * (size_t)NN);
+    _Float16* whEg2 = (_Float16*)alloc(sizeof(_Float16) * 12800);
+    _Float16* whEg3 = (_Float16*)alloc(sizeof(_Float16) * 4608);
+    _Float16* whDg2 = (_Float16*)alloc(sizeof(_Float16) * 5120);
+    _Float16* whDg3 = (_Float16*)alloc(sizeof(_Float16) * 15360);
 
     k_hist<<<NB_PART, 256, 0, stream>>>(dst, part_cnt);
     k_scanA<<<NPB, BS, 0, stream>>>(part_cnt, scan_out, bsums);
@@ -644,42 +753,22 @@
     k_part<<<NB_PART, 256, 0, stream>>>(src, dst, scan_out, epb);
     k_fine2<<<NBUCKET, 256, 0, stream>>>(bbase, epb, eidx, rowptr, dis);
 
-    k_wprep<160, 80><<<cdiv(160 * 80, 256), 256, 0, stream>>>(eg2_w, whEg2);
-    k_wprep<80, 40><<<cdiv(96 * 48, 256), 256, 0, stream>>>(eg3_w, whEg3);
-    k_wprep<40, 80><<<cdiv(64 * 80, 256), 256, 0, stream>>>(dg2_w, whDg2);
-    k_wprep<80, 160><<<cdiv(96 * 160, 256), 256, 0, stream>>>(dg3_w, whDg3);
-
-    k_scale3<<<cdiv(3LL * NN, BS), BS, 0, stream>>>(x, dis, bufB);
-    k_gather3d<0, false><<<cdiv(NN, BS), BS, 0, stream>>>(bufB, rowptr, eidx, dis, nullptr, bufA);
-    k_mm_rowbcast<3, 160, 1, 3><<<cdiv(NN * 40LL, BS), BS, 0, stream>>>(bufA, eg1_w, eg1_b, bufB);
-
-    k_mfma<160, 80, 0, false, 2><<<cdiv(NN, 64), 256, 0, stream>>>(
-        (const unsigned short*)bufB, whEg2, nullptr, G, dis);
-    k_gatherw<80, 1, true, true><<<cdiv(NN * 10LL, BS), BS, 0, stream>>>(G, rowptr, eidx, dis, eg2_b, bufA);
-
-    k_mfma<80, 40, 0, false, 2><<<cdiv(NN, 64), 256, 0, stream>>>(
-        (const unsigned short*)bufA, whEg3, nullptr, G, dis);
-    k_gatherw<40, 1, true, true><<<cdiv(NN * 5LL, BS), BS, 0, stream>>>(G, rowptr, eidx, dis, eg3_b, bufB);
-
-    k_mm_vec4<40, 20, 0, false, 2, true><<<cdiv((NN / 8) * 5LL, BS), BS, 0, stream>>>(
-        bufB, eg4_w, nullptr, (float*)G, dis);
-    k_gatherh<20, 1, true, true><<<cdiv(NN * 5LL, BS), BS, 0, stream>>>(G, rowptr, eidx, dis, eg4_b, bufA);
-
-    k_latent<<<cdiv(NN, 256), 256, 0, stream>>>((const unsigned short*)bufA,
-        el1_w, el1_b, el2_w, el2_b, dl1_w, dl1_b, dl2_w, dl2_b, dis, G);
-
-    k_gatherh<20, 0, false, true><<<cdiv(NN * 5LL, BS), BS, 0, stream>>>(G, rowptr, eidx, dis, nullptr, bufA);
-    k_mm_vec4<20, 40, 1, true, 2, true><<<cdiv((NN / 8) * 10LL, BS), BS, 0, stream>>>(
-        bufA, dg1_w, dg1_b, (float*)G, dis);
-
-    k_gatherw<40, 0, false, true><<<cdiv(NN * 5LL, BS), BS, 0, stream>>>(G, rowptr, eidx, dis, nullptr, bufB);
-    k_mfma<40, 80, 1, true, 2><<<cdiv(NN, 64), 256, 0, stream>>>(
-        (const unsigned short*)bufB, whDg2, dg2_b, G, dis);
-
-    k_gatherw<80, 0, false, true><<<cdiv(NN * 10LL, BS), BS, 0, stream>>>(G, rowptr, eidx, dis, nullptr, bufA);
-    k_mfma<80, 160, 1, true, 3><<<cdiv(NN, 64), 256, 0, stream>>>(
-        (const unsigned short*)bufA, whDg3, dg3_b, (unsigned short*)bufB, nullptr);
-
-    k_mm_vec<160, 3, 0, false, 1, true><<<cdiv((NN / 8) * 3LL, BS), BS, 0, stream>>>(bufB, dg4_w, nullptr, bufA, dis);
-    k_gather3d<2, true><<<cdiv(NN, BS), BS, 0, stream>>>(bufA, rowptr, eidx, dis, dg4_b, out);
-}
+    k_wprep_all<<<cdiv(37888, 256), 256, 0, stream>>>(eg2_w, eg3_w, dg2_w, dg3_w,
+                                                      whEg2, whEg3, whDg2, whDg3);
+
+    k_gather3x<<<cdiv(NN, BS), BS, 0, stream>>>(x, rowptr, eidx, dis, A3);
+    k_eg12<<<cdiv(NN, 64), 256, 0, stream>>>(A3, eg1_w, eg1_b, whEg2, GA, dis);
+    k_gmfma<80, 40, true, 1, false, 0, 2><<<cdiv(NN, 64), 256, 0, stream>>>(
+        GA, rowptr, eidx, dis, eg2_b, whEg3, nullptr, GB);
+    k_g40mm<<<cdiv(NN, 256), 256, 0, stream>>>(GB, rowptr, eidx, dis, eg3_b, eg4_w, GA);
+    k_g20_latent<<<cdiv(NN, 256), 256, 0, stream>>>(GA, rowptr, eidx, dis, eg4_b,
+        el1_w, el1_b, el2_w, el2_b, dl1_w, dl1_b, dl2_w, dl2_b, GB);
+    k_g20_mm<<<cdiv(NN, 256), 256, 0, stream>>>(GB, rowptr, eidx, dis, dg1_w, dg1_b, GA);
+    k_gmfma<40, 80, false, 0, true, 1, 2><<<cdiv(NN, 64), 256, 0, stream>>>(
+        GA, rowptr, eidx, dis, nullptr, whDg2, dg2_b, GB);
+    k_gmfma<80, 160, false, 0, true, 1, 3><<<cdiv(NN, 64), 256, 0, stream>>>(
+        GB, rowptr, eidx, dis, nullptr, whDg3, dg3_b, B160);
+    k_mm_vec<160, 3, 0, false, 1, true><<<cdiv((NN / 8) * 3LL, BS), BS, 0, stream>>>(
+        (const float*)B160, dg4_w, nullptr, A3, dis);
+    k_gather3d<2, true><<<cdiv(NN, BS), BS, 0, stream>>>(A3, rowptr, eidx, dis, dg4_b, out);
+}
```

Result: slower. 538.6 us (+2.1%).
